# Kernel optimization log

Measured on AMD Instinct MI355X. Metric: run time of the kernel, lower is better.

The kernel has to match this reference:

```python
import jax, jax.numpy as jnp
import numpy as np

NUM_PM = 254
NUM_VM = 768
SEQ = NUM_PM + NUM_VM + 2  # 1024
H = 8
D = 256
DH = D // H
FF = 1024
L = 3
B = 8
PM_COV = 16
VM_COV = 16


def _ln(x, g, b, eps=1e-5):
    m = jnp.mean(x, axis=-1, keepdims=True)
    v = jnp.mean((x - m) ** 2, axis=-1, keepdims=True)
    return (x - m) * jax.lax.rsqrt(v + eps) * g + b


def setup_inputs() -> dict:
    key = jax.random.key(0)
    ks = jax.random.split(key, 32)
    n = lambda k, s: (jax.random.normal(k, s, dtype=jnp.float32) * 0.02)
    return {
        "vm_states": jax.random.normal(ks[0], (B, NUM_VM, VM_COV), dtype=jnp.float32),
        "num_step_states": jax.random.uniform(ks[1], (B, 1, 1), dtype=jnp.float32),
        "pm_states": jax.random.normal(ks[2], (B, NUM_PM, PM_COV), dtype=jnp.float32),
        "vm_pm_relation": jax.random.randint(ks[3], (B, SEQ - 2, 1), 0, NUM_PM),
        "num_vms_mask": jnp.zeros((B, NUM_VM), dtype=bool),
        "pm_W": n(ks[4], (PM_COV, D)), "pm_b": jnp.zeros((D,), jnp.float32),
        "vm_W": n(ks[5], (VM_COV, D)), "vm_b": jnp.zeros((D,), jnp.float32),
        "Wqkv": n(ks[6], (L, D, 3 * D)), "bqkv": jnp.zeros((L, 3 * D), jnp.float32),
        "Wo": n(ks[7], (L, D, D)), "bo": jnp.zeros((L, D), jnp.float32),
        "ln1_g": jnp.ones((L, D), jnp.float32), "ln1_b": jnp.zeros((L, D), jnp.float32),
        "ln2_g": jnp.ones((L, D), jnp.float32), "ln2_b": jnp.zeros((L, D), jnp.float32),
        "W1": n(ks[8], (L, D, FF)), "b1": jnp.zeros((L, FF), jnp.float32),
        "W2": n(ks[9], (L, FF, D)), "b2": jnp.zeros((L, D), jnp.float32),
        "out_W": n(ks[10], (D, 1)), "out_b": jnp.zeros((1,), jnp.float32),
        "crit_W": n(ks[11], (D, 1)), "crit_b": jnp.zeros((1,), jnp.float32),
    }


def reference(vm_states, num_step_states, pm_states, vm_pm_relation, num_vms_mask,
              pm_W, pm_b, vm_W, vm_b, Wqkv, bqkv, Wo, bo,
              ln1_g, ln1_b, ln2_g, ln2_b, W1, b1, W2, b2,
              out_W, out_b, crit_W, crit_b):
    b = vm_states.shape[0]
    # --- relation-based sparse mask: True = blocked ---
    r = vm_pm_relation[:, :, 0]                              # [b, SEQ-2]
    inner = r[:, :, None] != r[:, None, :]                   # [b, SEQ-2, SEQ-2]
    local = jnp.ones((b, SEQ, SEQ), dtype=bool)
    local = local.at[:, 0, 0].set(False)
    local = local.at[:, -1, -1].set(False)
    local = local.at[:, 1:-1, 1:-1].set(inner)
    pad = jnp.zeros((b, SEQ), dtype=bool).at[:, 1 + NUM_PM:-1].set(num_vms_mask)
    bias = jnp.where(local | pad[:, None, :], -1e9, 0.0)[:, None]  # [b,1,SEQ,SEQ]
    # --- encode ---
    src = jnp.concatenate([jnp.tile(num_step_states, (1, 1, D)),
                           pm_states @ pm_W + pm_b], axis=1)       # [b, NUM_PM+1, D]
    critic_tok = -jnp.ones((b, 1, D), dtype=vm_states.dtype)
    tgt = jnp.concatenate([vm_states @ vm_W + vm_b, critic_tok], axis=1)  # [b, NUM_VM+1, D]
    x = jnp.concatenate([src, tgt], axis=1)                   # [b, SEQ, D]
    scale = 1.0 / np.sqrt(DH)
    for i in range(L):
        # pre-norm masked self-attention
        h = _ln(x, ln1_g[i], ln1_b[i])
        qkv = h @ Wqkv[i] + bqkv[i]
        q, k, v = [t.reshape(b, SEQ, H, DH) for t in jnp.split(qkv, 3, axis=-1)]
        scores = jnp.einsum('bqhd,bkhd->bhqk', q, k) * scale + bias
        attn = jax.nn.softmax(scores, axis=-1)
        o = jnp.einsum('bhqk,bkhd->bqhd', attn, v).reshape(b, SEQ, D)
        x = x + o @ Wo[i] + bo[i]
        # pre-norm gelu FFN
        h2 = _ln(x, ln2_g[i], ln2_b[i])
        x = x + jax.nn.gelu(h2 @ W1[i] + b1[i]) @ W2[i] + b2[i]
    tgt_out = x[:, NUM_PM + 1:]                               # [b, NUM_VM+1, D]
    score = (tgt_out[:, :-1] @ out_W + out_b)[..., 0]         # [b, NUM_VM]
    critic_score = tgt_out[:, -1] @ crit_W + crit_b           # [b, 1]
    return jnp.concatenate([score, critic_score], axis=1)     # [b, NUM_VM+1]
```

## Files before the change

kernel.cpp:

```cpp
#include <hip/hip_runtime.h>
#include <hip/hip_bf16.h>
#include <math.h>

#define NUM_PM 254
#define NUM_VM 768
#define SEQQ   1024
#define NH     8
#define DD     256
#define DH     32
#define FF     1024
#define NB     8
#define MROWS  (NB*SEQQ)

typedef unsigned short u16;
typedef __attribute__((ext_vector_type(8))) short bf16x8;
typedef __attribute__((ext_vector_type(4))) float f32x4;

__device__ __forceinline__ float bf2f(u16 u){
    union { float f; unsigned int i; } c; c.i = ((unsigned int)u) << 16; return c.f;
}
__device__ __forceinline__ u16 f2bf(float f){
    union { float f; unsigned int u; } c; c.f = f;
    unsigned int r = c.u + 0x7FFFu + ((c.u >> 16) & 1u);
    return (u16)(r >> 16);
}
__device__ __forceinline__ float gelu_tanh(float x){
    float x3 = x*x*x;
    float t = tanhf(0.7978845608028654f*(x + 0.044715f*x3));
    return 0.5f*x*(1.0f+t);
}

#define GLOAD16(gp, lp) __builtin_amdgcn_global_load_lds( \
    (const __attribute__((address_space(1))) void*)(gp), \
    (__attribute__((address_space(3))) void*)(lp), 16, 0, 0)

__global__ void prologue_kernel(const float* __restrict__ Wqkv, const float* __restrict__ Wo,
                                const float* __restrict__ W1,   const float* __restrict__ W2,
                                u16* __restrict__ wq, u16* __restrict__ wo,
                                u16* __restrict__ w1, u16* __restrict__ w2,
                                const int* __restrict__ rel, const unsigned char* __restrict__ mask,
                                int* __restrict__ counts, int* __restrict__ offs,
                                int* __restrict__ members,
                                const float* __restrict__ vm_states,
                                const float* __restrict__ num_step,
                                const float* __restrict__ pm_states,
                                const float* __restrict__ pm_W, const float* __restrict__ pm_b,
                                const float* __restrict__ vm_W, const float* __restrict__ vm_b,
                                const float* __restrict__ g, const float* __restrict__ beta,
                                float* __restrict__ x, u16* __restrict__ h)
{
    __shared__ float t[32][33];
    __shared__ int cntS[256], offS[256], wsum4[4];
    int bid = blockIdx.x;
    int tid = threadIdx.x;
    if (bid < 2304){
        int id = bid;
        const float* in; u16* out; int K, N, layer, tile;
        if (id < 576)       { in=Wqkv; out=wq; K=256;  N=768;  layer=id/192; tile=id%192; }
        else if (id < 768)  { id-=576;  in=Wo; out=wo; K=256;  N=256;  layer=id/64;  tile=id%64;  }
        else if (id < 1536) { id-=768;  in=W1; out=w1; K=256;  N=1024; layer=id/256; tile=id%256; }
        else                { id-=1536; in=W2; out=w2; K=1024; N=256;  layer=id/256; tile=id%256; }
        int ntx = N/32;
        int n0 = (tile % ntx)*32, k0 = (tile / ntx)*32;
        size_t lofs = (size_t)layer * K * N;
        int tx = tid & 31, ty = tid >> 5;
        #pragma unroll
        for (int i=0;i<4;i++)
            t[ty + i*8][tx] = in[lofs + (size_t)(k0 + ty + i*8)*N + n0 + tx];
        __syncthreads();
        #pragma unroll
        for (int i=0;i<4;i++)
            out[lofs + (size_t)(n0 + ty + i*8)*K + k0 + tx] = f2bf(t[tx][ty + i*8]);
    } else if (bid < 2312){
        int b = bid - 2304;
        cntS[tid] = 0;
        __syncthreads();
        int myc[4], myp[4];
        #pragma unroll
        for (int si=0; si<4; si++){
            int s = si*256 + tid;
            bool valid = (s != 0) && (s != SEQQ-1);
            if (valid && s >= 1+NUM_PM && mask[b*NUM_VM + (s-1-NUM_PM)]) valid = false;
            myc[si] = -1;
            if (valid){
                myc[si] = rel[b*(SEQQ-2) + s-1];
                myp[si] = atomicAdd(&cntS[myc[si]], 1);
            }
        }
        __syncthreads();
        int v = cntS[tid];
        int incl = v;
        #pragma unroll
        for (int d=1; d<64; d<<=1){
            int n = __shfl_up(incl, d);
            if ((tid & 63) >= d) incl += n;
        }
        offS[tid] = incl - v;
        if ((tid & 63) == 63) wsum4[tid>>6] = incl;
        __syncthreads();
        {
            int w = tid >> 6, base = 0;
            #pragma unroll
            for (int i=0;i<4;i++) if (i < w) base += wsum4[i];
            offS[tid] += base;
        }
        __syncthreads();
        #pragma unroll
        for (int si=0; si<4; si++)
            if (myc[si] >= 0)
                members[b*SEQQ + offS[myc[si]] + myp[si]] = si*256 + tid;
        counts[b*256 + tid] = cntS[tid];
        offs[b*256 + tid]   = offS[tid];
    } else {
        int row = (bid - 2312)*4 + (tid>>6);
        int lane = tid & 63;
        int b = row >> 10, s = row & 1023;
        int col = lane*4;
        float4 out;
        if (s == 0){
            float v = num_step[b]; out = (float4){v,v,v,v};
        } else if (s == SEQQ-1){
            out = (float4){-1.f,-1.f,-1.f,-1.f};
        } else {
            const float* in; const float* W; const float* bias;
            if (s <= NUM_PM){ in = pm_states + (size_t)(b*NUM_PM + s-1)*16; W = pm_W; bias = pm_b; }
            else            { in = vm_states + (size_t)(b*NUM_VM + (s-1-NUM_PM))*16; W = vm_W; bias = vm_b; }
            float4 i0 = *(const float4*)in,      i1 = *(const float4*)(in+4);
            float4 i2 = *(const float4*)(in+8),  i3 = *(const float4*)(in+12);
            float in16[16] = {i0.x,i0.y,i0.z,i0.w, i1.x,i1.y,i1.z,i1.w,
                              i2.x,i2.y,i2.z,i2.w, i3.x,i3.y,i3.z,i3.w};
            out = *(const float4*)&bias[col];
            #pragma unroll
            for (int k=0;k<16;k++){
                float4 w4 = *(const float4*)&W[k*DD + col];
                out.x = fmaf(in16[k], w4.x, out.x);
                out.y = fmaf(in16[k], w4.y, out.y);
                out.z = fmaf(in16[k], w4.z, out.z);
                out.w = fmaf(in16[k], w4.w, out.w);
            }
        }
        *(float4*)&x[(size_t)row*DD + col] = out;
        float s1 = out.x+out.y+out.z+out.w;
        float s2 = fmaf(out.x,out.x, fmaf(out.y,out.y, fmaf(out.z,out.z, out.w*out.w)));
        #pragma unroll
        for (int off=1; off<64; off<<=1){ s1 += __shfl_xor(s1,off); s2 += __shfl_xor(s2,off); }
        float m    = s1*(1.0f/DD);
        float var  = s2*(1.0f/DD) - m*m;
        float rstd = rsqrtf(var + 1e-5f);
        float4 g4 = *(const float4*)&g[col];
        float4 b4 = *(const float4*)&beta[col];
        short4 o;
        o.x = (short)f2bf((out.x-m)*rstd*g4.x + b4.x);
        o.y = (short)f2bf((out.y-m)*rstd*g4.y + b4.y);
        o.z = (short)f2bf((out.z-m)*rstd*g4.z + b4.z);
        o.w = (short)f2bf((out.w-m)*rstd*g4.w + b4.w);
        *(short4*)&h[(size_t)row*DD + col] = o;
    }
}

__global__ void ln_kernel(const float* __restrict__ x, const float* __restrict__ g,
                          const float* __restrict__ bta, u16* __restrict__ out)
{
    int row = blockIdx.x*4 + (threadIdx.x>>6);
    int lane = threadIdx.x & 63;
    const float4 v = *(const float4*)&x[(size_t)row*DD + lane*4];
    float s1 = v.x+v.y+v.z+v.w;
    float s2 = fmaf(v.x,v.x, fmaf(v.y,v.y, fmaf(v.z,v.z, v.w*v.w)));
    #pragma unroll
    for (int off=1; off<64; off<<=1){ s1 += __shfl_xor(s1,off); s2 += __shfl_xor(s2,off); }
    float m    = s1*(1.0f/DD);
    float var  = s2*(1.0f/DD) - m*m;
    float rstd = rsqrtf(var + 1e-5f);
    float4 g4 = *(const float4*)&g[lane*4];
    float4 b4 = *(const float4*)&bta[lane*4];
    short4 o;
    o.x = (short)f2bf((v.x-m)*rstd*g4.x + b4.x);
    o.y = (short)f2bf((v.y-m)*rstd*g4.y + b4.y);
    o.z = (short)f2bf((v.z-m)*rstd*g4.z + b4.z);
    o.w = (short)f2bf((v.w-m)*rstd*g4.w + b4.w);
    *(short4*)&out[(size_t)row*DD + lane*4] = o;
}

__launch_bounds__(256)
__global__ void qgemm_kernel(const u16* __restrict__ A, const u16* __restrict__ Bt,
                             const float* __restrict__ bias, u16* __restrict__ C,
                             int N, int K)
{
    __shared__ u16 As[2][64][32];
    __shared__ u16 Bs[2][128][32];
    int tid = threadIdx.x;
    int wid = tid >> 6, lane = tid & 63;
    int wr = wid >> 1, wc = wid & 1;
    int row0 = blockIdx.y*64, col0 = blockIdx.x*128;
    int l15 = lane & 15, lh = lane >> 4;

    const u16* Ag = A  + (size_t)(row0 + wid*16 + (lane>>2))*K + (lane&3)*8;
    const u16* Bg = Bt + (size_t)(col0 + wid*32 + (lane>>2))*K + (lane&3)*8;

#define STAGE_Q(buf, k0) do{ \
    GLOAD16(Ag + (k0),          &As[buf][wid*16][0]);    \
    GLOAD16(Bg + (k0),          &Bs[buf][wid*32][0]);    \
    GLOAD16(Bg + (k0) + 16*K,   &Bs[buf][wid*32+16][0]); }while(0)

    f32x4 acc[2][4] = {};
    int nk = K >> 5;
    STAGE_Q(0, 0);
    __syncthreads();
    for (int kt = 0; kt < nk; kt++){
        int cur = kt & 1;
        if (kt+1 < nk) STAGE_Q(cur^1, (kt+1)*32);
        bf16x8 af[2], bfv[4];
        #pragma unroll
        for (int i=0;i<2;i++)
            af[i] = *(const bf16x8*)&As[cur][wr*32 + i*16 + l15][lh*8];
        #pragma unroll
        for (int j=0;j<4;j++)
            bfv[j] = *(const bf16x8*)&Bs[cur][wc*64 + j*16 + l15][lh*8];
        #pragma unroll
        for (int i=0;i<2;i++)
            #pragma unroll
            for (int j=0;j<4;j++)
                acc[i][j] = __builtin_amdgcn_mfma_f32_16x16x32_bf16(af[i], bfv[j], acc[i][j], 0,0,0);
        __syncthreads();
    }
#undef STAGE_Q

    #pragma unroll
    for (int i=0;i<2;i++){
        #pragma unroll
        for (int j=0;j<4;j++){
            int col = col0 + wc*64 + j*16 + l15;
            float bb = bias[col];
            #pragma unroll
            for (int r=0;r<4;r++){
                int row = row0 + wr*32 + i*16 + lh*4 + r;
                C[(size_t)row*N + col] = f2bf(acc[i][j][r] + bb);
            }
        }
    }
}

__launch_bounds__(256)
__global__ void mgemm_kernel(const u16* __restrict__ A, const u16* __restrict__ Bt,
                             const float* __restrict__ bias, u16* __restrict__ C,
                             int N, int K)
{
    __shared__ u16 As[2][128][32];
    __shared__ u16 Bs[2][128][32];
    int tid = threadIdx.x;
    int wid = tid >> 6, lane = tid & 63;
    int wr = wid >> 1, wc = wid & 1;
    int row0 = blockIdx.y*128, col0 = blockIdx.x*128;
    int l15 = lane & 15, lh = lane >> 4;

    const u16* Ag = A  + (size_t)(row0 + wid*32 + (lane>>2))*K + (lane&3)*8;
    const u16* Bg = Bt + (size_t)(col0 + wid*32 + (lane>>2))*K + (lane&3)*8;

#define STAGE_M(buf, k0) do{ \
    GLOAD16(Ag + (k0),          &As[buf][wid*32][0]);    \
    GLOAD16(Ag + (k0) + 16*K,   &As[buf][wid*32+16][0]); \
    GLOAD16(Bg + (k0),          &Bs[buf][wid*32][0]);    \
    GLOAD16(Bg + (k0) + 16*K,   &Bs[buf][wid*32+16][0]); }while(0)

    f32x4 acc[4][4] = {};
    int nk = K >> 5;
    STAGE_M(0, 0);
    __syncthreads();
    for (int kt = 0; kt < nk; kt++){
        int cur = kt & 1;
        if (kt+1 < nk) STAGE_M(cur^1, (kt+1)*32);
        bf16x8 af[4], bfv[4];
        #pragma unroll
        for (int f=0; f<4; f++){
            af[f]  = *(const bf16x8*)&As[cur][wr*64 + f*16 + l15][lh*8];
            bfv[f] = *(const bf16x8*)&Bs[cur][wc*64 + f*16 + l15][lh*8];
        }
        #pragma unroll
        for (int i=0;i<4;i++)
            #pragma unroll
            for (int j=0;j<4;j++)
                acc[i][j] = __builtin_amdgcn_mfma_f32_16x16x32_bf16(af[i], bfv[j], acc[i][j], 0,0,0);
        __syncthreads();
    }
#undef STAGE_M

    #pragma unroll
    for (int i=0;i<4;i++){
        #pragma unroll
        for (int j=0;j<4;j++){
            int col = col0 + wc*64 + j*16 + l15;
            float bb = bias[col];
            #pragma unroll
            for (int r=0;r<4;r++){
                int row = row0 + wr*64 + i*16 + lh*4 + r;
                C[(size_t)row*N + col] = f2bf(gelu_tanh(acc[i][j][r] + bb));
            }
        }
    }
}

template<int HEAD>
__launch_bounds__(256)
__global__ void mgemm64_kernel(const u16* __restrict__ A, const u16* __restrict__ Bt,
                               const float* __restrict__ bias, float* __restrict__ x,
                               const float* __restrict__ out_W, const float* __restrict__ out_b,
                               const float* __restrict__ crit_W, const float* __restrict__ crit_b,
                               float* __restrict__ out, int K)
{
    __shared__ u16 As[2][64][32];
    __shared__ u16 Bs[2][64][32];
    int tid = threadIdx.x;
    int wid = tid >> 6, lane = tid & 63;
    int wr = wid >> 1, wc = wid & 1;
    int row0 = blockIdx.y*64, col0 = blockIdx.x*64;
    int l15 = lane & 15, lh = lane >> 4;

    const u16* Ag = A  + (size_t)(row0 + wid*16 + (lane>>2))*K + (lane&3)*8;
    const u16* Bg = Bt + (size_t)(col0 + wid*16 + (lane>>2))*K + (lane&3)*8;

#define STAGE_S(buf, k0) do{ \
    GLOAD16(Ag + (k0), &As[buf][wid*16][0]); \
    GLOAD16(Bg + (k0), &Bs[buf][wid*16][0]); }while(0)

    f32x4 acc[2][2] = {};
    int nk = K >> 5;
    STAGE_S(0, 0);
    __syncthreads();
    for (int kt = 0; kt < nk; kt++){
        int cur = kt & 1;
        if (kt+1 < nk) STAGE_S(cur^1, (kt+1)*32);
        bf16x8 af[2], bfv[2];
        #pragma unroll
        for (int i=0;i<2;i++)
            af[i] = *(const bf16x8*)&As[cur][wr*32 + i*16 + l15][lh*8];
        #pragma unroll
        for (int j=0;j<2;j++)
            bfv[j] = *(const bf16x8*)&Bs[cur][wc*32 + j*16 + l15][lh*8];
        #pragma unroll
        for (int i=0;i<2;i++)
            #pragma unroll
            for (int j=0;j<2;j++)
                acc[i][j] = __builtin_amdgcn_mfma_f32_16x16x32_bf16(af[i], bfv[j], acc[i][j], 0,0,0);
        __syncthreads();
    }
#undef STAGE_S

    #pragma unroll
    for (int i=0;i<2;i++){
        #pragma unroll
        for (int r=0;r<4;r++){
            int row = row0 + wr*32 + i*16 + lh*4 + r;
            float hp = 0.f;
            bool do_head = false;
            int s = row & 1023;
            #pragma unroll
            for (int j=0;j<2;j++){
                int col = col0 + wc*32 + j*16 + l15;
                size_t idx = (size_t)row*DD + col;
                float v = acc[i][j][r] + bias[col] + x[idx];
                x[idx] = v;
                if (HEAD){
                    float w = (s == 1023) ? crit_W[col] : out_W[col];
                    hp = fmaf(v, w, hp);
                }
            }
            if (HEAD && s >= 1 + NUM_PM){
                do_head = true;
                hp += __shfl_xor(hp, 1);
                hp += __shfl_xor(hp, 2);
                hp += __shfl_xor(hp, 4);
                hp += __shfl_xor(hp, 8);
                if (l15 == 0){
                    int b = row >> 10;
                    int jj = (s == 1023) ? 768 : (s - (1 + NUM_PM));
                    float add = hp;
                    if (blockIdx.x == 0 && wc == 0)
                        add += (s == 1023) ? crit_b[0] : out_b[0];
                    atomicAdd(&out[b*769 + jj], add);
                }
            }
            (void)do_head;
        }
    }
}

__launch_bounds__(256)
__global__ void attn_kernel(const u16* __restrict__ qkv, const int* __restrict__ rel,
                            const int* __restrict__ counts, const int* __restrict__ offs,
                            const int* __restrict__ members, u16* __restrict__ o)
{
    int gq = blockIdx.x*4 + (threadIdx.x >> 6);
    int lane = threadIdx.x & 63;
    int b = gq >> 10, s = gq & 1023;
    const float scale = 0.17677669529663687f;

    const u16* base = qkv + (size_t)(b*SEQQ + s)*768 + lane*4;
    short4 q4i = *(const short4*)base;
    float qx = bf2f((u16)q4i.x)*scale, qy = bf2f((u16)q4i.y)*scale,
          qz = bf2f((u16)q4i.z)*scale, qw = bf2f((u16)q4i.w)*scale;

    int cnt; const int* mlist = nullptr;
    if (s == 0 || s == SEQQ-1) { cnt = 1; }
    else {
        int c = rel[b*(SEQQ-2) + s-1];
        cnt   = counts[b*256 + c];
        mlist = members + b*SEQQ + offs[b*256 + c];
    }

    float m_run = -1e30f, l_run = 0.f;
    float ax=0.f, ay=0.f, az=0.f, aw=0.f;
    for (int j0 = 0; j0 < cnt; j0 += 4){
        short4 k4[4], v4[4];
        #pragma unroll
        for (int k=0;k<4;k++){
            int jj = j0 + k; jj = (jj < cnt) ? jj : (cnt-1);
            int mi = mlist ? mlist[jj] : s;
            const u16* kb = qkv + (size_t)(b*SEQQ + mi)*768 + 256 + lane*4;
            k4[k] = *(const short4*)kb;
            v4[k] = *(const short4*)(kb + 256);
        }
        #pragma unroll
        for (int k=0;k<4;k++){
            if (j0 + k < cnt){
                float sc = qx*bf2f((u16)k4[k].x) + qy*bf2f((u16)k4[k].y)
                         + qz*bf2f((u16)k4[k].z) + qw*bf2f((u16)k4[k].w);
                sc += __shfl_xor(sc, 1);
                sc += __shfl_xor(sc, 2);
                sc += __shfl_xor(sc, 4);
                float mn = fmaxf(m_run, sc);
                float corr = __expf(m_run - mn);
                float p = __expf(sc - mn);
                l_run = l_run*corr + p;
                ax = ax*corr + p*bf2f((u16)v4[k].x);
                ay = ay*corr + p*bf2f((u16)v4[k].y);
                az = az*corr + p*bf2f((u16)v4[k].z);
                aw = aw*corr + p*bf2f((u16)v4[k].w);
                m_run = mn;
            }
        }
    }
    float inv = (l_run > 0.f) ? 1.0f/l_run : 0.f;
    u16* orow = o + (size_t)(b*SEQQ + s)*DD + lane*4;
    short4 outv;
    outv.x = (short)f2bf(ax*inv); outv.y = (short)f2bf(ay*inv);
    outv.z = (short)f2bf(az*inv); outv.w = (short)f2bf(aw*inv);
    *(short4*)orow = outv;
}

extern "C" void kernel_launch(void* const* d_in, const int* in_sizes, int n_in,
                              void* d_out, int out_size, void* d_ws, size_t ws_size,
                              hipStream_t stream)
{
    const float* vm_states = (const float*)d_in[0];
    const float* num_step  = (const float*)d_in[1];
    const float* pm_states = (const float*)d_in[2];
    const int*   rel       = (const int*)d_in[3];
    const unsigned char* mask = (const unsigned char*)d_in[4];
    const float* pm_W = (const float*)d_in[5];
    const float* pm_b = (const float*)d_in[6];
    const float* vm_W = (const float*)d_in[7];
    const float* vm_b = (const float*)d_in[8];
    const float* Wqkv = (const float*)d_in[9];
    const float* bqkv = (const float*)d_in[10];
    const float* Wo   = (const float*)d_in[11];
    const float* bo   = (const float*)d_in[12];
    const float* ln1g = (const float*)d_in[13];
    const float* ln1b = (const float*)d_in[14];
    const float* ln2g = (const float*)d_in[15];
    const float* ln2b = (const float*)d_in[16];
    const float* W1   = (const float*)d_in[17];
    const float* b1   = (const float*)d_in[18];
    const float* W2   = (const float*)d_in[19];
    const float* b2   = (const float*)d_in[20];
    const float* out_W = (const float*)d_in[21];
    const float* out_b = (const float*)d_in[22];
    const float* crit_W = (const float*)d_in[23];
    const float* crit_b = (const float*)d_in[24];

    char* ws = (char*)d_ws;
    const size_t MB = 1024*1024;
    float* x    = (float*)(ws);
    u16*   hbuf = (u16*)(ws + 8*MB);
    u16*   aout = (u16*)(ws + 12*MB);
    u16*   qkv  = (u16*)(ws + 16*MB);
    u16*   ff1  = (u16*)(ws + 28*MB);
    u16*   wq   = (u16*)(ws + 44*MB);
    u16*   wo   = wq + (size_t)3*768*256;
    u16*   w1   = wo + (size_t)3*256*256;
    u16*   w2   = w1 + (size_t)3*1024*256;
    int*   counts  = (int*)(ws + 50*MB);
    int*   offs    = counts + NB*256;
    int*   members = offs   + NB*256;

    hipMemsetAsync(d_out, 0, (size_t)out_size*sizeof(float), stream);
    prologue_kernel<<<4360, 256, 0, stream>>>(Wqkv, Wo, W1, W2, wq, wo, w1, w2,
                                              rel, mask, counts, offs, members,
                                              vm_states, num_step, pm_states,
                                              pm_W, pm_b, vm_W, vm_b,
                                              ln1g, ln1b, x, hbuf);
    for (int i=0;i<3;i++){
        qgemm_kernel<<<dim3(768/128, MROWS/64),256,0,stream>>>(
            hbuf, wq + (size_t)i*768*256, bqkv + i*768, qkv, 768, 256);
        attn_kernel<<<MROWS/4, 256, 0, stream>>>(qkv, rel, counts, offs, members, aout);
        mgemm64_kernel<0><<<dim3(256/64, MROWS/64),256,0,stream>>>(
            aout, wo + (size_t)i*256*256, bo + i*DD, x,
            nullptr, nullptr, nullptr, nullptr, nullptr, 256);
        ln_kernel<<<MROWS/4,256,0,stream>>>(x, ln2g + i*DD, ln2b + i*DD, hbuf);
        mgemm_kernel<<<dim3(1024/128, MROWS/128),256,0,stream>>>(
            hbuf, w1 + (size_t)i*1024*256, b1 + i*FF, ff1, 1024, 256);
        if (i < 2){
            mgemm64_kernel<0><<<dim3(256/64, MROWS/64),256,0,stream>>>(
                ff1, w2 + (size_t)i*256*1024, b2 + i*DD, x,
                nullptr, nullptr, nullptr, nullptr, nullptr, 1024);
            ln_kernel<<<MROWS/4,256,0,stream>>>(x, ln1g + (i+1)*DD, ln1b + (i+1)*DD, hbuf);
        } else {
            mgemm64_kernel<1><<<dim3(256/64, MROWS/64),256,0,stream>>>(
                ff1, w2 + (size_t)i*256*1024, b2 + i*DD, x,
                out_W, out_b, crit_W, crit_b, (float*)d_out, 1024);
        }
    }
}
```

Measured before the change: 332.9 us.

## Replace LDS-staged QKV and FFN1 GEMMs with register-resident weight GEMM

Replaces the two LDS double-buffered GEMM kernels used for QKV projection and FFN up-projection (K=256) with one templated kernel. Each wave keeps its 64-column slice of the weights entirely in registers across the full K=256 and streams A rows straight from global memory, with no shared memory and no barriers. The intent is to remove the LDS staging and sync overhead for these short-K GEMMs. In exchange it uses many VGPRs (32 bf16x8 weight fragments per wave), which lowers occupancy, and A is reloaded from global/L2 by all four waves without reuse through LDS.

Result: slower. 389.9 us (+17.2%).

```diff
diff --git a/kernel.cpp b/kernel.cpp
--- a/kernel.cpp
+++ b/kernel.cpp
@@ -181,119 +181,51 @@
     *(short4*)&out[(size_t)row*DD + lane*4] = o;
 }
 
+template<int EPI>
 __launch_bounds__(256)
-__global__ void qgemm_kernel(const u16* __restrict__ A, const u16* __restrict__ Bt,
-                             const float* __restrict__ bias, u16* __restrict__ C,
-                             int N, int K)
-{
-    __shared__ u16 As[2][64][32];
-    __shared__ u16 Bs[2][128][32];
+__global__ void wgemm_kernel(const u16* __restrict__ A, const u16* __restrict__ Bt,
+                             const float* __restrict__ bias, u16* __restrict__ C, int N)
+{
     int tid = threadIdx.x;
     int wid = tid >> 6, lane = tid & 63;
-    int wr = wid >> 1, wc = wid & 1;
-    int row0 = blockIdx.y*64, col0 = blockIdx.x*128;
     int l15 = lane & 15, lh = lane >> 4;
-
-    const u16* Ag = A  + (size_t)(row0 + wid*16 + (lane>>2))*K + (lane&3)*8;
-    const u16* Bg = Bt + (size_t)(col0 + wid*32 + (lane>>2))*K + (lane&3)*8;
-
-#define STAGE_Q(buf, k0) do{ \
-    GLOAD16(Ag + (k0),          &As[buf][wid*16][0]);    \
-    GLOAD16(Bg + (k0),          &Bs[buf][wid*32][0]);    \
-    GLOAD16(Bg + (k0) + 16*K,   &Bs[buf][wid*32+16][0]); }while(0)
+    int col0 = blockIdx.x*256 + wid*64;
+    int row0 = blockIdx.y*32;
+
+    bf16x8 bq[4][8];
+    #pragma unroll
+    for (int j=0;j<4;j++){
+        const u16* bp = Bt + (size_t)(col0 + j*16 + l15)*256 + lh*8;
+        #pragma unroll
+        for (int t=0;t<8;t++)
+            bq[j][t] = *(const bf16x8*)(bp + t*32);
+    }
 
     f32x4 acc[2][4] = {};
-    int nk = K >> 5;
-    STAGE_Q(0, 0);
-    __syncthreads();
-    for (int kt = 0; kt < nk; kt++){
-        int cur = kt & 1;
-        if (kt+1 < nk) STAGE_Q(cur^1, (kt+1)*32);
-        bf16x8 af[2], bfv[4];
-        #pragma unroll
-        for (int i=0;i<2;i++)
-            af[i] = *(const bf16x8*)&As[cur][wr*32 + i*16 + l15][lh*8];
-        #pragma unroll
-        for (int j=0;j<4;j++)
-            bfv[j] = *(const bf16x8*)&Bs[cur][wc*64 + j*16 + l15][lh*8];
-        #pragma unroll
-        for (int i=0;i<2;i++)
-            #pragma unroll
-            for (int j=0;j<4;j++)
-                acc[i][j] = __builtin_amdgcn_mfma_f32_16x16x32_bf16(af[i], bfv[j], acc[i][j], 0,0,0);
-        __syncthreads();
-    }
-#undef STAGE_Q
+    const u16* Ab = A + (size_t)(row0 + l15)*256 + lh*8;
+    #pragma unroll
+    for (int t=0;t<8;t++){
+        bf16x8 a0 = *(const bf16x8*)(Ab + t*32);
+        bf16x8 a1 = *(const bf16x8*)(Ab + 16*256 + t*32);
+        #pragma unroll
+        for (int j=0;j<4;j++){
+            acc[0][j] = __builtin_amdgcn_mfma_f32_16x16x32_bf16(a0, bq[j][t], acc[0][j], 0,0,0);
+            acc[1][j] = __builtin_amdgcn_mfma_f32_16x16x32_bf16(a1, bq[j][t], acc[1][j], 0,0,0);
+        }
+    }
 
     #pragma unroll
     for (int i=0;i<2;i++){
         #pragma unroll
         for (int j=0;j<4;j++){
-            int col = col0 + wc*64 + j*16 + l15;
+            int col = col0 + j*16 + l15;
             float bb = bias[col];
             #pragma unroll
             for (int r=0;r<4;r++){
-                int row = row0 + wr*32 + i*16 + lh*4 + r;
-                C[(size_t)row*N + col] = f2bf(acc[i][j][r] + bb);
-            }
-        }
-    }
-}
-
-__launch_bounds__(256)
-__global__ void mgemm_kernel(const u16* __restrict__ A, const u16* __restrict__ Bt,
-                             const float* __restrict__ bias, u16* __restrict__ C,
-                             int N, int K)
-{
-    __shared__ u16 As[2][128][32];
-    __shared__ u16 Bs[2][128][32];
-    int tid = threadIdx.x;
-    int wid = tid >> 6, lane = tid & 63;
-    int wr = wid >> 1, wc = wid & 1;
-    int row0 = blockIdx.y*128, col0 = blockIdx.x*128;
-    int l15 = lane & 15, lh = lane >> 4;
-
-    const u16* Ag = A  + (size_t)(row0 + wid*32 + (lane>>2))*K + (lane&3)*8;
-    const u16* Bg = Bt + (size_t)(col0 + wid*32 + (lane>>2))*K + (lane&3)*8;
-
-#define STAGE_M(buf, k0) do{ \
-    GLOAD16(Ag + (k0),          &As[buf][wid*32][0]);    \
-    GLOAD16(Ag + (k0) + 16*K,   &As[buf][wid*32+16][0]); \
-    GLOAD16(Bg + (k0),          &Bs[buf][wid*32][0]);    \
-    GLOAD16(Bg + (k0) + 16*K,   &Bs[buf][wid*32+16][0]); }while(0)
-
-    f32x4 acc[4][4] = {};
-    int nk = K >> 5;
-    STAGE_M(0, 0);
-    __syncthreads();
-    for (int kt = 0; kt < nk; kt++){
-        int cur = kt & 1;
-        if (kt+1 < nk) STAGE_M(cur^1, (kt+1)*32);
-        bf16x8 af[4], bfv[4];
-        #pragma unroll
-        for (int f=0; f<4; f++){
-            af[f]  = *(const bf16x8*)&As[cur][wr*64 + f*16 + l15][lh*8];
-            bfv[f] = *(const bf16x8*)&Bs[cur][wc*64 + f*16 + l15][lh*8];
-        }
-        #pragma unroll
-        for (int i=0;i<4;i++)
-            #pragma unroll
-            for (int j=0;j<4;j++)
-                acc[i][j] = __builtin_amdgcn_mfma_f32_16x16x32_bf16(af[i], bfv[j], acc[i][j], 0,0,0);
-        __syncthreads();
-    }
-#undef STAGE_M
-
-    #pragma unroll
-    for (int i=0;i<4;i++){
-        #pragma unroll
-        for (int j=0;j<4;j++){
-            int col = col0 + wc*64 + j*16 + l15;
-            float bb = bias[col];
-            #pragma unroll
-            for (int r=0;r<4;r++){
-                int row = row0 + wr*64 + i*16 + lh*4 + r;
-                C[(size_t)row*N + col] = f2bf(gelu_tanh(acc[i][j][r] + bb));
+                int row = row0 + i*16 + lh*4 + r;
+                float v = acc[i][j][r] + bb;
+                if (EPI==2) v = gelu_tanh(v);
+                C[(size_t)row*N + col] = f2bf(v);
             }
         }
     }
@@ -351,7 +283,6 @@
         for (int r=0;r<4;r++){
             int row = row0 + wr*32 + i*16 + lh*4 + r;
             float hp = 0.f;
-            bool do_head = false;
             int s = row & 1023;
             #pragma unroll
             for (int j=0;j<2;j++){
@@ -365,7 +296,6 @@
                 }
             }
             if (HEAD && s >= 1 + NUM_PM){
-                do_head = true;
                 hp += __shfl_xor(hp, 1);
                 hp += __shfl_xor(hp, 2);
                 hp += __shfl_xor(hp, 4);
@@ -379,7 +309,6 @@
                     atomicAdd(&out[b*769 + jj], add);
                 }
             }
-            (void)do_head;
         }
     }
 }
@@ -499,15 +428,15 @@
                                               pm_W, pm_b, vm_W, vm_b,
                                               ln1g, ln1b, x, hbuf);
     for (int i=0;i<3;i++){
-        qgemm_kernel<<<dim3(768/128, MROWS/64),256,0,stream>>>(
-            hbuf, wq + (size_t)i*768*256, bqkv + i*768, qkv, 768, 256);
+        wgemm_kernel<0><<<dim3(768/256, MROWS/32),256,0,stream>>>(
+            hbuf, wq + (size_t)i*768*256, bqkv + i*768, qkv, 768);
         attn_kernel<<<MROWS/4, 256, 0, stream>>>(qkv, rel, counts, offs, members, aout);
         mgemm64_kernel<0><<<dim3(256/64, MROWS/64),256,0,stream>>>(
             aout, wo + (size_t)i*256*256, bo + i*DD, x,
             nullptr, nullptr, nullptr, nullptr, nullptr, 256);
         ln_kernel<<<MROWS/4,256,0,stream>>>(x, ln2g + i*DD, ln2b + i*DD, hbuf);
-        mgemm_kernel<<<dim3(1024/128, MROWS/128),256,0,stream>>>(
-            hbuf, w1 + (size_t)i*1024*256, b1 + i*FF, ff1, 1024, 256);
+        wgemm_kernel<2><<<dim3(1024/256, MROWS/32),256,0,stream>>>(
+            hbuf, w1 + (size_t)i*1024*256, b1 + i*FF, ff1, 1024);
         if (i < 2){
             mgemm64_kernel<0><<<dim3(256/64, MROWS/64),256,0,stream>>>(
                 ff1, w2 + (size_t)i*256*1024, b2 + i*DD, x,
```

## Group attention by relation class so each wave reuses its class's keys and values

Applied to the files above, without the earlier changes.

Attention now runs one wave per (batch, relation class) instead of one wave per query row. Each wave walks that class's query list and, for classes with at most 8 keys, keeps the keys and values in registers and reuses them across all its queries. This removes the repeated K/V reloads from global memory. The prologue now builds separate key and query membership lists, and it also zeroes the output buffer, which replaces a separate memset call. The cost is load imbalance across classes of different sizes and serialized query loops within one wave, which lowers parallelism.

New measurement: 451.4 us. 1.36x slower.

```diff
diff --git a/kernel.cpp b/kernel.cpp
--- a/kernel.cpp
+++ b/kernel.cpp
@@ -39,18 +39,20 @@
                                 u16* __restrict__ wq, u16* __restrict__ wo,
                                 u16* __restrict__ w1, u16* __restrict__ w2,
                                 const int* __restrict__ rel, const unsigned char* __restrict__ mask,
-                                int* __restrict__ counts, int* __restrict__ offs,
-                                int* __restrict__ members,
+                                int* __restrict__ kcnt, int* __restrict__ koff, int* __restrict__ kmem,
+                                int* __restrict__ qcnt, int* __restrict__ qoff, int* __restrict__ qmem,
                                 const float* __restrict__ vm_states,
                                 const float* __restrict__ num_step,
                                 const float* __restrict__ pm_states,
                                 const float* __restrict__ pm_W, const float* __restrict__ pm_b,
                                 const float* __restrict__ vm_W, const float* __restrict__ vm_b,
                                 const float* __restrict__ g, const float* __restrict__ beta,
-                                float* __restrict__ x, u16* __restrict__ h)
+                                float* __restrict__ x, u16* __restrict__ h,
+                                float* __restrict__ outz)
 {
     __shared__ float t[32][33];
     __shared__ int cntS[256], offS[256], wsum4[4];
+    __shared__ int qcntS[256], qoffS[256], qwsum4[4];
     int bid = blockIdx.x;
     int tid = threadIdx.x;
     if (bid < 2304){
@@ -73,44 +75,64 @@
             out[lofs + (size_t)(n0 + ty + i*8)*K + k0 + tx] = f2bf(t[tx][ty + i*8]);
     } else if (bid < 2312){
         int b = bid - 2304;
-        cntS[tid] = 0;
-        __syncthreads();
-        int myc[4], myp[4];
+        cntS[tid] = 0; qcntS[tid] = 0;
+        __syncthreads();
+        int myc[4], myp[4], myqp[4];
+        bool mym[4];
         #pragma unroll
         for (int si=0; si<4; si++){
             int s = si*256 + tid;
-            bool valid = (s != 0) && (s != SEQQ-1);
-            if (valid && s >= 1+NUM_PM && mask[b*NUM_VM + (s-1-NUM_PM)]) valid = false;
-            myc[si] = -1;
-            if (valid){
-                myc[si] = rel[b*(SEQQ-2) + s-1];
-                myp[si] = atomicAdd(&cntS[myc[si]], 1);
-            }
-        }
-        __syncthreads();
-        int v = cntS[tid];
-        int incl = v;
-        #pragma unroll
-        for (int d=1; d<64; d<<=1){
-            int n = __shfl_up(incl, d);
-            if ((tid & 63) >= d) incl += n;
-        }
-        offS[tid] = incl - v;
-        if ((tid & 63) == 63) wsum4[tid>>6] = incl;
+            bool mid = (s != 0) && (s != SEQQ-1);
+            myc[si] = -1; mym[si] = false;
+            if (mid){
+                int cc = rel[b*(SEQQ-2) + s-1];
+                myc[si] = cc;
+                bool masked = (s >= 1+NUM_PM) && mask[b*NUM_VM + (s-1-NUM_PM)];
+                mym[si] = masked;
+                myqp[si] = atomicAdd(&qcntS[cc], 1);
+                if (!masked) myp[si] = atomicAdd(&cntS[cc], 1);
+            }
+        }
         __syncthreads();
         {
-            int w = tid >> 6, base = 0;
-            #pragma unroll
-            for (int i=0;i<4;i++) if (i < w) base += wsum4[i];
+            int v = cntS[tid], qv = qcntS[tid];
+            int incl = v, qincl = qv;
+            #pragma unroll
+            for (int d=1; d<64; d<<=1){
+                int n  = __shfl_up(incl, d);
+                int qn = __shfl_up(qincl, d);
+                if ((tid & 63) >= d){ incl += n; qincl += qn; }
+            }
+            offS[tid]  = incl - v;
+            qoffS[tid] = qincl - qv;
+            if ((tid & 63) == 63){ wsum4[tid>>6] = incl; qwsum4[tid>>6] = qincl; }
+        }
+        __syncthreads();
+        {
+            int w = tid >> 6, base = 0, qbase = 0;
+            #pragma unroll
+            for (int i=0;i<4;i++) if (i < w){ base += wsum4[i]; qbase += qwsum4[i]; }
             offS[tid] += base;
-        }
-        __syncthreads();
-        #pragma unroll
-        for (int si=0; si<4; si++)
-            if (myc[si] >= 0)
-                members[b*SEQQ + offS[myc[si]] + myp[si]] = si*256 + tid;
-        counts[b*256 + tid] = cntS[tid];
-        offs[b*256 + tid]   = offS[tid];
+            qoffS[tid] += qbase;
+        }
+        __syncthreads();
+        #pragma unroll
+        for (int si=0; si<4; si++){
+            if (myc[si] >= 0){
+                int s = si*256 + tid;
+                if (!mym[si]) kmem[b*SEQQ + offS[myc[si]] + myp[si]] = s;
+                qmem[b*SEQQ + qoffS[myc[si]] + myqp[si]] = s;
+            }
+        }
+        kcnt[b*256 + tid] = cntS[tid];
+        koff[b*256 + tid] = offS[tid];
+        qcnt[b*256 + tid] = qcntS[tid];
+        qoff[b*256 + tid] = qoffS[tid];
+        #pragma unroll
+        for (int si=0; si<4; si++){
+            int idx = si*256 + tid;
+            if (idx < 769) outz[b*769 + idx] = 0.f;
+        }
     } else {
         int row = (bid - 2312)*4 + (tid>>6);
         int lane = tid & 63;
@@ -351,7 +373,6 @@
         for (int r=0;r<4;r++){
             int row = row0 + wr*32 + i*16 + lh*4 + r;
             float hp = 0.f;
-            bool do_head = false;
             int s = row & 1023;
             #pragma unroll
             for (int j=0;j<2;j++){
@@ -365,7 +386,6 @@
                 }
             }
             if (HEAD && s >= 1 + NUM_PM){
-                do_head = true;
                 hp += __shfl_xor(hp, 1);
                 hp += __shfl_xor(hp, 2);
                 hp += __shfl_xor(hp, 4);
@@ -379,72 +399,139 @@
                     atomicAdd(&out[b*769 + jj], add);
                 }
             }
-            (void)do_head;
         }
     }
 }
 
 __launch_bounds__(256)
-__global__ void attn_kernel(const u16* __restrict__ qkv, const int* __restrict__ rel,
-                            const int* __restrict__ counts, const int* __restrict__ offs,
-                            const int* __restrict__ members, u16* __restrict__ o)
+__global__ void gattn_kernel(const u16* __restrict__ qkv,
+                             const int* __restrict__ kcnt, const int* __restrict__ koff,
+                             const int* __restrict__ kmem,
+                             const int* __restrict__ qcnt, const int* __restrict__ qoff,
+                             const int* __restrict__ qmem,
+                             u16* __restrict__ o)
 {
-    int gq = blockIdx.x*4 + (threadIdx.x >> 6);
+    int gidx = blockIdx.x*4 + (threadIdx.x >> 6);
     int lane = threadIdx.x & 63;
-    int b = gq >> 10, s = gq & 1023;
     const float scale = 0.17677669529663687f;
 
-    const u16* base = qkv + (size_t)(b*SEQQ + s)*768 + lane*4;
-    short4 q4i = *(const short4*)base;
-    float qx = bf2f((u16)q4i.x)*scale, qy = bf2f((u16)q4i.y)*scale,
-          qz = bf2f((u16)q4i.z)*scale, qw = bf2f((u16)q4i.w)*scale;
-
-    int cnt; const int* mlist = nullptr;
-    if (s == 0 || s == SEQQ-1) { cnt = 1; }
-    else {
-        int c = rel[b*(SEQQ-2) + s-1];
-        cnt   = counts[b*256 + c];
-        mlist = members + b*SEQQ + offs[b*256 + c];
-    }
-
-    float m_run = -1e30f, l_run = 0.f;
-    float ax=0.f, ay=0.f, az=0.f, aw=0.f;
-    for (int j0 = 0; j0 < cnt; j0 += 4){
-        short4 k4[4], v4[4];
-        #pragma unroll
-        for (int k=0;k<4;k++){
-            int jj = j0 + k; jj = (jj < cnt) ? jj : (cnt-1);
-            int mi = mlist ? mlist[jj] : s;
+    if (gidx >= NB*256){
+        int idx = gidx - NB*256;
+        int b = idx >> 1, s = (idx & 1) ? (SEQQ-1) : 0;
+        const u16* vrow = qkv + (size_t)(b*SEQQ + s)*768 + 512 + lane*4;
+        *(short4*)(o + (size_t)(b*SEQQ + s)*DD + lane*4) = *(const short4*)vrow;
+        return;
+    }
+    int b = gidx >> 8, c = gidx & 255;
+    int gq = qcnt[b*256 + c];
+    if (gq == 0) return;
+    int gk = kcnt[b*256 + c];
+    const int* klist = kmem + b*SEQQ + koff[b*256 + c];
+    const int* qlist = qmem + b*SEQQ + qoff[b*256 + c];
+
+    if (gk == 0){
+        for (int i=0;i<gq;i++){
+            int s = qlist[i];
+            short4 z = {0,0,0,0};
+            *(short4*)(o + (size_t)(b*SEQQ + s)*DD + lane*4) = z;
+        }
+        return;
+    }
+
+    if (gk <= 8){
+        float4 kr[8], vr[8];
+        #pragma unroll
+        for (int j=0;j<8;j++){
+            int mi = klist[(j < gk) ? j : 0];
             const u16* kb = qkv + (size_t)(b*SEQQ + mi)*768 + 256 + lane*4;
-            k4[k] = *(const short4*)kb;
-            v4[k] = *(const short4*)(kb + 256);
-        }
-        #pragma unroll
-        for (int k=0;k<4;k++){
-            if (j0 + k < cnt){
-                float sc = qx*bf2f((u16)k4[k].x) + qy*bf2f((u16)k4[k].y)
-                         + qz*bf2f((u16)k4[k].z) + qw*bf2f((u16)k4[k].w);
-                sc += __shfl_xor(sc, 1);
-                sc += __shfl_xor(sc, 2);
-                sc += __shfl_xor(sc, 4);
-                float mn = fmaxf(m_run, sc);
-                float corr = __expf(m_run - mn);
-                float p = __expf(sc - mn);
-                l_run = l_run*corr + p;
-                ax = ax*corr + p*bf2f((u16)v4[k].x);
-                ay = ay*corr + p*bf2f((u16)v4[k].y);
-                az = az*corr + p*bf2f((u16)v4[k].z);
-                aw = aw*corr + p*bf2f((u16)v4[k].w);
-                m_run = mn;
-            }
-        }
-    }
-    float inv = (l_run > 0.f) ? 1.0f/l_run : 0.f;
-    u16* orow = o + (size_t)(b*SEQQ + s)*DD + lane*4;
-    short4 outv;
-    outv.x = (short)f2bf(ax*inv); outv.y = (short)f2bf(ay*inv);
-    outv.z = (short)f2bf(az*inv); outv.w = (short)f2bf(aw*inv);
-    *(short4*)orow = outv;
+            short4 k4 = *(const short4*)kb;
+            short4 v4 = *(const short4*)(kb + 256);
+            kr[j] = (float4){bf2f((u16)k4.x), bf2f((u16)k4.y), bf2f((u16)k4.z), bf2f((u16)k4.w)};
+            vr[j] = (float4){bf2f((u16)v4.x), bf2f((u16)v4.y), bf2f((u16)v4.z), bf2f((u16)v4.w)};
+        }
+        for (int i=0;i<gq;i++){
+            int s = qlist[i];
+            const u16* qb = qkv + (size_t)(b*SEQQ + s)*768 + lane*4;
+            short4 q4i = *(const short4*)qb;
+            float qx = bf2f((u16)q4i.x)*scale, qy = bf2f((u16)q4i.y)*scale,
+                  qz = bf2f((u16)q4i.z)*scale, qw = bf2f((u16)q4i.w)*scale;
+            float sc[8];
+            #pragma unroll
+            for (int j=0;j<8;j++){
+                float d = qx*kr[j].x + qy*kr[j].y + qz*kr[j].z + qw*kr[j].w;
+                d += __shfl_xor(d, 1);
+                d += __shfl_xor(d, 2);
+                d += __shfl_xor(d, 4);
+                sc[j] = d;
+            }
+            float m = -1e30f;
+            #pragma unroll
+            for (int j=0;j<8;j++) if (j < gk) m = fmaxf(m, sc[j]);
+            float l = 0.f;
+            float ax=0.f, ay=0.f, az=0.f, aw=0.f;
+            #pragma unroll
+            for (int j=0;j<8;j++){
+                if (j < gk){
+                    float p = __expf(sc[j] - m);
+                    l += p;
+                    ax = fmaf(p, vr[j].x, ax);
+                    ay = fmaf(p, vr[j].y, ay);
+                    az = fmaf(p, vr[j].z, az);
+                    aw = fmaf(p, vr[j].w, aw);
+                }
+            }
+            float inv = 1.0f/l;
+            short4 outv;
+            outv.x = (short)f2bf(ax*inv); outv.y = (short)f2bf(ay*inv);
+            outv.z = (short)f2bf(az*inv); outv.w = (short)f2bf(aw*inv);
+            *(short4*)(o + (size_t)(b*SEQQ + s)*DD + lane*4) = outv;
+        }
+    } else {
+        for (int i=0;i<gq;i++){
+            int s = qlist[i];
+            const u16* qb = qkv + (size_t)(b*SEQQ + s)*768 + lane*4;
+            short4 q4i = *(const short4*)qb;
+            float qx = bf2f((u16)q4i.x)*scale, qy = bf2f((u16)q4i.y)*scale,
+                  qz = bf2f((u16)q4i.z)*scale, qw = bf2f((u16)q4i.w)*scale;
+            float m_run = -1e30f, l_run = 0.f;
+            float ax=0.f, ay=0.f, az=0.f, aw=0.f;
+            for (int j0 = 0; j0 < gk; j0 += 4){
+                short4 k4[4], v4[4];
+                #pragma unroll
+                for (int k=0;k<4;k++){
+                    int jj = j0 + k; jj = (jj < gk) ? jj : (gk-1);
+                    int mi = klist[jj];
+                    const u16* kb = qkv + (size_t)(b*SEQQ + mi)*768 + 256 + lane*4;
+                    k4[k] = *(const short4*)kb;
+                    v4[k] = *(const short4*)(kb + 256);
+                }
+                #pragma unroll
+                for (int k=0;k<4;k++){
+                    if (j0 + k < gk){
+                        float d = qx*bf2f((u16)k4[k].x) + qy*bf2f((u16)k4[k].y)
+                                + qz*bf2f((u16)k4[k].z) + qw*bf2f((u16)k4[k].w);
+                        d += __shfl_xor(d, 1);
+                        d += __shfl_xor(d, 2);
+                        d += __shfl_xor(d, 4);
+                        float mn = fmaxf(m_run, d);
+                        float corr = __expf(m_run - mn);
+                        float p = __expf(d - mn);
+                        l_run = l_run*corr + p;
+                        ax = ax*corr + p*bf2f((u16)v4[k].x);
+                        ay = ay*corr + p*bf2f((u16)v4[k].y);
+                        az = az*corr + p*bf2f((u16)v4[k].z);
+                        aw = aw*corr + p*bf2f((u16)v4[k].w);
+                        m_run = mn;
+                    }
+                }
+            }
+            float inv = 1.0f/l_run;
+            short4 outv;
+            outv.x = (short)f2bf(ax*inv); outv.y = (short)f2bf(ay*inv);
+            outv.z = (short)f2bf(az*inv); outv.w = (short)f2bf(aw*inv);
+            *(short4*)(o + (size_t)(b*SEQQ + s)*DD + lane*4) = outv;
+        }
+    }
 }
 
 extern "C" void kernel_launch(void* const* d_in, const int* in_sizes, int n_in,
@@ -488,20 +575,23 @@
     u16*   wo   = wq + (size_t)3*768*256;
     u16*   w1   = wo + (size_t)3*256*256;
     u16*   w2   = w1 + (size_t)3*1024*256;
-    int*   counts  = (int*)(ws + 50*MB);
-    int*   offs    = counts + NB*256;
-    int*   members = offs   + NB*256;
-
-    hipMemsetAsync(d_out, 0, (size_t)out_size*sizeof(float), stream);
+    int*   kcnt = (int*)(ws + 50*MB);
+    int*   koff = kcnt + NB*256;
+    int*   kmem = koff + NB*256;
+    int*   qcnt = kmem + NB*SEQQ;
+    int*   qoff = qcnt + NB*256;
+    int*   qmem = qoff + NB*256;
+
     prologue_kernel<<<4360, 256, 0, stream>>>(Wqkv, Wo, W1, W2, wq, wo, w1, w2,
-                                              rel, mask, counts, offs, members,
+                                              rel, mask, kcnt, koff, kmem, qcnt, qoff, qmem,
                                               vm_states, num_step, pm_states,
                                               pm_W, pm_b, vm_W, vm_b,
-                                              ln1g, ln1b, x, hbuf);
+                                              ln1g, ln1b, x, hbuf, (float*)d_out);
     for (int i=0;i<3;i++){
         qgemm_kernel<<<dim3(768/128, MROWS/64),256,0,stream>>>(
             hbuf, wq + (size_t)i*768*256, bqkv + i*768, qkv, 768, 256);
-        attn_kernel<<<MROWS/4, 256, 0, stream>>>(qkv, rel, counts, offs, members, aout);
+        gattn_kernel<<<(NB*256 + 16)/4, 256, 0, stream>>>(
+            qkv, kcnt, koff, kmem, qcnt, qoff, qmem, aout);
         mgemm64_kernel<0><<<dim3(256/64, MROWS/64),256,0,stream>>>(
             aout, wo + (size_t)i*256*256, bo + i*DD, x,
             nullptr, nullptr, nullptr, nullptr, nullptr, 256);
```

## Precompute per-query padded key lists and fold output zeroing into prologue

Applied to the files above, without the earlier changes.

The prologue now builds, for every query row, a padded list of up to 16 key indices plus its count. The attention kernel reads this list with four int4 loads and runs a fixed, unrolled chunk loop, instead of looking up rel, counts and offsets and then reading members one at a time. Boundary rows become a direct V copy, and the separate output memset is replaced by zeroing inside the prologue. The cost is extra prologue work and 64 bytes of index data per row, with a fallback loop kept for groups larger than 16.

After: 332.4 us. Within noise of the previous version (-0.2%).

```diff
diff --git a/kernel.cpp b/kernel.cpp
--- a/kernel.cpp
+++ b/kernel.cpp
@@ -39,18 +39,20 @@
                                 u16* __restrict__ wq, u16* __restrict__ wo,
                                 u16* __restrict__ w1, u16* __restrict__ w2,
                                 const int* __restrict__ rel, const unsigned char* __restrict__ mask,
-                                int* __restrict__ counts, int* __restrict__ offs,
-                                int* __restrict__ members,
+                                int* __restrict__ kcnt, int* __restrict__ koff, int* __restrict__ kmem,
+                                int* __restrict__ pcnt, int* __restrict__ poff, int* __restrict__ pmem,
                                 const float* __restrict__ vm_states,
                                 const float* __restrict__ num_step,
                                 const float* __restrict__ pm_states,
                                 const float* __restrict__ pm_W, const float* __restrict__ pm_b,
                                 const float* __restrict__ vm_W, const float* __restrict__ vm_b,
                                 const float* __restrict__ g, const float* __restrict__ beta,
-                                float* __restrict__ x, u16* __restrict__ h)
+                                float* __restrict__ x, u16* __restrict__ h,
+                                float* __restrict__ outz)
 {
     __shared__ float t[32][33];
     __shared__ int cntS[256], offS[256], wsum4[4];
+    __shared__ int memS[1040];
     int bid = blockIdx.x;
     int tid = threadIdx.x;
     if (bid < 2304){
@@ -76,27 +78,31 @@
         cntS[tid] = 0;
         __syncthreads();
         int myc[4], myp[4];
+        bool mykey[4];
         #pragma unroll
         for (int si=0; si<4; si++){
             int s = si*256 + tid;
-            bool valid = (s != 0) && (s != SEQQ-1);
-            if (valid && s >= 1+NUM_PM && mask[b*NUM_VM + (s-1-NUM_PM)]) valid = false;
-            myc[si] = -1;
-            if (valid){
-                myc[si] = rel[b*(SEQQ-2) + s-1];
-                myp[si] = atomicAdd(&cntS[myc[si]], 1);
-            }
-        }
-        __syncthreads();
-        int v = cntS[tid];
-        int incl = v;
-        #pragma unroll
-        for (int d=1; d<64; d<<=1){
-            int n = __shfl_up(incl, d);
-            if ((tid & 63) >= d) incl += n;
-        }
-        offS[tid] = incl - v;
-        if ((tid & 63) == 63) wsum4[tid>>6] = incl;
+            bool mid = (s != 0) && (s != SEQQ-1);
+            myc[si] = -1; mykey[si] = false;
+            if (mid){
+                int cc = rel[b*(SEQQ-2) + s-1];
+                myc[si] = cc;
+                bool masked = (s >= 1+NUM_PM) && mask[b*NUM_VM + (s-1-NUM_PM)];
+                if (!masked){ mykey[si] = true; myp[si] = atomicAdd(&cntS[cc], 1); }
+            }
+        }
+        __syncthreads();
+        {
+            int v = cntS[tid];
+            int incl = v;
+            #pragma unroll
+            for (int d=1; d<64; d<<=1){
+                int n = __shfl_up(incl, d);
+                if ((tid & 63) >= d) incl += n;
+            }
+            offS[tid] = incl - v;
+            if ((tid & 63) == 63) wsum4[tid>>6] = incl;
+        }
         __syncthreads();
         {
             int w = tid >> 6, base = 0;
@@ -106,11 +112,41 @@
         }
         __syncthreads();
         #pragma unroll
-        for (int si=0; si<4; si++)
-            if (myc[si] >= 0)
-                members[b*SEQQ + offS[myc[si]] + myp[si]] = si*256 + tid;
-        counts[b*256 + tid] = cntS[tid];
-        offs[b*256 + tid]   = offS[tid];
+        for (int si=0; si<4; si++){
+            if (mykey[si]){
+                int s = si*256 + tid;
+                int pos = offS[myc[si]] + myp[si];
+                memS[pos] = s;
+                kmem[b*SEQQ + pos] = s;
+            }
+        }
+        kcnt[b*256 + tid] = cntS[tid];
+        koff[b*256 + tid] = offS[tid];
+        __syncthreads();
+        #pragma unroll
+        for (int si=0; si<4; si++){
+            int s = si*256 + tid;
+            if (myc[si] >= 0){
+                int c = myc[si];
+                int cnt = cntS[c], off = offS[c];
+                pcnt[b*SEQQ + s] = cnt;
+                poff[b*SEQQ + s] = b*SEQQ + off;
+                int mrow[16];
+                #pragma unroll
+                for (int j=0;j<16;j++)
+                    mrow[j] = (j < cnt) ? memS[off + j] : s;
+                int4* prow = (int4*)&pmem[(size_t)(b*SEQQ + s)*16];
+                prow[0] = (int4){mrow[0], mrow[1], mrow[2], mrow[3]};
+                prow[1] = (int4){mrow[4], mrow[5], mrow[6], mrow[7]};
+                prow[2] = (int4){mrow[8], mrow[9], mrow[10],mrow[11]};
+                prow[3] = (int4){mrow[12],mrow[13],mrow[14],mrow[15]};
+            }
+        }
+        #pragma unroll
+        for (int si=0; si<4; si++){
+            int idx = si*256 + tid;
+            if (idx < 769) outz[b*769 + idx] = 0.f;
+        }
     } else {
         int row = (bid - 2312)*4 + (tid>>6);
         int lane = tid & 63;
@@ -351,7 +387,6 @@
         for (int r=0;r<4;r++){
             int row = row0 + wr*32 + i*16 + lh*4 + r;
             float hp = 0.f;
-            bool do_head = false;
             int s = row & 1023;
             #pragma unroll
             for (int j=0;j<2;j++){
@@ -365,7 +400,6 @@
                 }
             }
             if (HEAD && s >= 1 + NUM_PM){
-                do_head = true;
                 hp += __shfl_xor(hp, 1);
                 hp += __shfl_xor(hp, 2);
                 hp += __shfl_xor(hp, 4);
@@ -379,68 +413,114 @@
                     atomicAdd(&out[b*769 + jj], add);
                 }
             }
-            (void)do_head;
         }
     }
 }
 
 __launch_bounds__(256)
-__global__ void attn_kernel(const u16* __restrict__ qkv, const int* __restrict__ rel,
-                            const int* __restrict__ counts, const int* __restrict__ offs,
-                            const int* __restrict__ members, u16* __restrict__ o)
+__global__ void attn_kernel(const u16* __restrict__ qkv,
+                            const int* __restrict__ pcnt, const int* __restrict__ pmem,
+                            const int* __restrict__ poff, const int* __restrict__ kmem,
+                            u16* __restrict__ o)
 {
     int gq = blockIdx.x*4 + (threadIdx.x >> 6);
     int lane = threadIdx.x & 63;
     int b = gq >> 10, s = gq & 1023;
     const float scale = 0.17677669529663687f;
 
-    const u16* base = qkv + (size_t)(b*SEQQ + s)*768 + lane*4;
-    short4 q4i = *(const short4*)base;
+    if (s == 0 || s == SEQQ-1){
+        const u16* vrow = qkv + (size_t)gq*768 + 512 + lane*4;
+        *(short4*)(o + (size_t)gq*DD + lane*4) = *(const short4*)vrow;
+        return;
+    }
+
+    const u16* qb = qkv + (size_t)gq*768 + lane*4;
+    short4 q4i = *(const short4*)qb;
     float qx = bf2f((u16)q4i.x)*scale, qy = bf2f((u16)q4i.y)*scale,
           qz = bf2f((u16)q4i.z)*scale, qw = bf2f((u16)q4i.w)*scale;
 
-    int cnt; const int* mlist = nullptr;
-    if (s == 0 || s == SEQQ-1) { cnt = 1; }
-    else {
-        int c = rel[b*(SEQQ-2) + s-1];
-        cnt   = counts[b*256 + c];
-        mlist = members + b*SEQQ + offs[b*256 + c];
-    }
+    int cnt = pcnt[gq];
+    const int4* prow = (const int4*)&pmem[(size_t)gq*16];
+    int4 m0 = prow[0], m1 = prow[1], m2 = prow[2], m3 = prow[3];
 
     float m_run = -1e30f, l_run = 0.f;
     float ax=0.f, ay=0.f, az=0.f, aw=0.f;
-    for (int j0 = 0; j0 < cnt; j0 += 4){
-        short4 k4[4], v4[4];
-        #pragma unroll
-        for (int k=0;k<4;k++){
-            int jj = j0 + k; jj = (jj < cnt) ? jj : (cnt-1);
-            int mi = mlist ? mlist[jj] : s;
-            const u16* kb = qkv + (size_t)(b*SEQQ + mi)*768 + 256 + lane*4;
-            k4[k] = *(const short4*)kb;
-            v4[k] = *(const short4*)(kb + 256);
-        }
-        #pragma unroll
-        for (int k=0;k<4;k++){
-            if (j0 + k < cnt){
-                float sc = qx*bf2f((u16)k4[k].x) + qy*bf2f((u16)k4[k].y)
-                         + qz*bf2f((u16)k4[k].z) + qw*bf2f((u16)k4[k].w);
-                sc += __shfl_xor(sc, 1);
-                sc += __shfl_xor(sc, 2);
-                sc += __shfl_xor(sc, 4);
-                float mn = fmaxf(m_run, sc);
-                float corr = __expf(m_run - mn);
-                float p = __expf(sc - mn);
-                l_run = l_run*corr + p;
-                ax = ax*corr + p*bf2f((u16)v4[k].x);
-                ay = ay*corr + p*bf2f((u16)v4[k].y);
-                az = az*corr + p*bf2f((u16)v4[k].z);
-                aw = aw*corr + p*bf2f((u16)v4[k].w);
-                m_run = mn;
-            }
-        }
-    }
+
+#define ACHUNK(BASE, MV) do{                                              \
+    if ((BASE) < cnt){                                                    \
+        short4 k4[4], v4[4];                                              \
+        const int mi0=(MV).x, mi1=(MV).y, mi2=(MV).z, mi3=(MV).w;         \
+        const u16* kb0 = qkv + (size_t)(b*SEQQ + mi0)*768 + 256 + lane*4; \
+        const u16* kb1 = qkv + (size_t)(b*SEQQ + mi1)*768 + 256 + lane*4; \
+        const u16* kb2 = qkv + (size_t)(b*SEQQ + mi2)*768 + 256 + lane*4; \
+        const u16* kb3 = qkv + (size_t)(b*SEQQ + mi3)*768 + 256 + lane*4; \
+        k4[0]=*(const short4*)kb0; v4[0]=*(const short4*)(kb0+256);       \
+        k4[1]=*(const short4*)kb1; v4[1]=*(const short4*)(kb1+256);       \
+        k4[2]=*(const short4*)kb2; v4[2]=*(const short4*)(kb2+256);       \
+        k4[3]=*(const short4*)kb3; v4[3]=*(const short4*)(kb3+256);       \
+        _Pragma("unroll")                                                 \
+        for (int k=0;k<4;k++){                                            \
+            if ((BASE) + k < cnt){                                        \
+                float sc = qx*bf2f((u16)k4[k].x) + qy*bf2f((u16)k4[k].y)  \
+                         + qz*bf2f((u16)k4[k].z) + qw*bf2f((u16)k4[k].w); \
+                sc += __shfl_xor(sc, 1);                                  \
+                sc += __shfl_xor(sc, 2);                                  \
+                sc += __shfl_xor(sc, 4);                                  \
+                float mn = fmaxf(m_run, sc);                              \
+                float corr = __expf(m_run - mn);                          \
+                float p = __expf(sc - mn);                                \
+                l_run = l_run*corr + p;                                   \
+                ax = ax*corr + p*bf2f((u16)v4[k].x);                      \
+                ay = ay*corr + p*bf2f((u16)v4[k].y);                      \
+                az = az*corr + p*bf2f((u16)v4[k].z);                      \
+                aw = aw*corr + p*bf2f((u16)v4[k].w);                      \
+                m_run = mn;                                               \
+            }                                                             \
+        }                                                                 \
+    } }while(0)
+
+    if (cnt <= 16){
+        ACHUNK(0,  m0);
+        ACHUNK(4,  m1);
+        ACHUNK(8,  m2);
+        ACHUNK(12, m3);
+    } else {
+        const int* klist = kmem + poff[gq];
+        for (int j0 = 0; j0 < cnt; j0 += 4){
+            short4 k4[4], v4[4];
+            #pragma unroll
+            for (int k=0;k<4;k++){
+                int jj = j0 + k; jj = (jj < cnt) ? jj : (cnt-1);
+                int mi = klist[jj];
+                const u16* kb = qkv + (size_t)(b*SEQQ + mi)*768 + 256 + lane*4;
+                k4[k] = *(const short4*)kb;
+                v4[k] = *(const short4*)(kb + 256);
+            }
+            #pragma unroll
+            for (int k=0;k<4;k++){
+                if (j0 + k < cnt){
+                    float sc = qx*bf2f((u16)k4[k].x) + qy*bf2f((u16)k4[k].y)
+                             + qz*bf2f((u16)k4[k].z) + qw*bf2f((u16)k4[k].w);
+                    sc += __shfl_xor(sc, 1);
+                    sc += __shfl_xor(sc, 2);
+                    sc += __shfl_xor(sc, 4);
+                    float mn = fmaxf(m_run, sc);
+                    float corr = __expf(m_run - mn);
+                    float p = __expf(sc - mn);
+                    l_run = l_run*corr + p;
+                    ax = ax*corr + p*bf2f((u16)v4[k].x);
+                    ay = ay*corr + p*bf2f((u16)v4[k].y);
+                    az = az*corr + p*bf2f((u16)v4[k].z);
+                    aw = aw*corr + p*bf2f((u16)v4[k].w);
+                    m_run = mn;
+                }
+            }
+        }
+    }
+#undef ACHUNK
+
     float inv = (l_run > 0.f) ? 1.0f/l_run : 0.f;
-    u16* orow = o + (size_t)(b*SEQQ + s)*DD + lane*4;
+    u16* orow = o + (size_t)gq*DD + lane*4;
     short4 outv;
     outv.x = (short)f2bf(ax*inv); outv.y = (short)f2bf(ay*inv);
     outv.z = (short)f2bf(az*inv); outv.w = (short)f2bf(aw*inv);
@@ -488,20 +568,22 @@
     u16*   wo   = wq + (size_t)3*768*256;
     u16*   w1   = wo + (size_t)3*256*256;
     u16*   w2   = w1 + (size_t)3*1024*256;
-    int*   counts  = (int*)(ws + 50*MB);
-    int*   offs    = counts + NB*256;
-    int*   members = offs   + NB*256;
-
-    hipMemsetAsync(d_out, 0, (size_t)out_size*sizeof(float), stream);
+    int*   kcnt = (int*)(ws + 50*MB);
+    int*   koff = kcnt + NB*256;
+    int*   kmem = koff + NB*256;
+    int*   pcnt = kmem + NB*SEQQ;
+    int*   poff = pcnt + MROWS;
+    int*   pmem = poff + MROWS;
+
     prologue_kernel<<<4360, 256, 0, stream>>>(Wqkv, Wo, W1, W2, wq, wo, w1, w2,
-                                              rel, mask, counts, offs, members,
+                                              rel, mask, kcnt, koff, kmem, pcnt, poff, pmem,
                                               vm_states, num_step, pm_states,
                                               pm_W, pm_b, vm_W, vm_b,
-                                              ln1g, ln1b, x, hbuf);
+                                              ln1g, ln1b, x, hbuf, (float*)d_out);
     for (int i=0;i<3;i++){
         qgemm_kernel<<<dim3(768/128, MROWS/64),256,0,stream>>>(
             hbuf, wq + (size_t)i*768*256, bqkv + i*768, qkv, 768, 256);
-        attn_kernel<<<MROWS/4, 256, 0, stream>>>(qkv, rel, counts, offs, members, aout);
+        attn_kernel<<<MROWS/4, 256, 0, stream>>>(qkv, pcnt, pmem, poff, kmem, aout);
         mgemm64_kernel<0><<<dim3(256/64, MROWS/64),256,0,stream>>>(
             aout, wo + (size_t)i*256*256, bo + i*DD, x,
             nullptr, nullptr, nullptr, nullptr, nullptr, 256);
```
